# Kernel optimization log

Measured on AMD Instinct MI355X. Metric: run time of the kernel, lower is better.

## Reference

```python
import jax, jax.numpy as jnp
import numpy as np

B, S, C = 4, 2048, 2048
D = C // 4  # head dim = 512

def setup_inputs() -> dict:
    key = jax.random.key(0)
    k1, k2, k3, k4, k5 = jax.random.split(key, 5)
    scale = 1.0 / np.sqrt(C)
    return {
        "x": jax.random.normal(k1, (B, S, C), dtype=jnp.float32),
        "Wqkv": jax.random.normal(k2, (3 * D, C), dtype=jnp.float32) * scale,
        "bqkv": jax.random.normal(k3, (3 * D,), dtype=jnp.float32) * 0.01,
        "Wo": jax.random.normal(k4, (C, D), dtype=jnp.float32) * (1.0 / np.sqrt(D)),
        "bo": jax.random.normal(k5, (C,), dtype=jnp.float32) * 0.01,
    }

def reference(x, Wqkv, bqkv, Wo, bo):
    Bx, Sx, Cx = x.shape
    d = Cx // 4
    # fused QKV projection: [B,S,3d] -> split into q,k,v each [B,S,d]
    qkv = jnp.einsum('bsc,oc->bso', x, Wqkv) + bqkv
    qkv = qkv.reshape(Bx, Sx, 3, d)
    q, k, v = qkv[:, :, 0], qkv[:, :, 1], qkv[:, :, 2]
    # scaled dot-product attention (full [B,S,S] scores, as in original)
    attn = jnp.einsum('bqd,bkd->bqk', q, k) / jnp.sqrt(jnp.asarray(d, x.dtype))
    attn = jax.nn.softmax(attn, axis=-1)
    ctx = jnp.einsum('bqk,bkd->bqd', attn, v)
    # output projection d -> C
    return jnp.einsum('bsd,od->bso', ctx, Wo) + bo
```

## Files before the change

kernel.cpp:

```cpp
#include <hip/hip_runtime.h>
#include <math.h>


typedef __bf16 bf16;
typedef bf16 bf16x8 __attribute__((ext_vector_type(8)));
typedef bf16 bf16x4 __attribute__((ext_vector_type(4)));
typedef float f32x4 __attribute__((ext_vector_type(4)));

#define BB 4
#define SS 2048
#define CC 2048
#define DD 512
#define ND3 1536
#define MM 8192

typedef const __attribute__((address_space(1))) unsigned int g_u32;
typedef __attribute__((address_space(3))) unsigned int l_u32;

__device__ __forceinline__ void gl_lds16(const bf16* g, bf16* l) {
    __builtin_amdgcn_global_load_lds((g_u32*)g, (l_u32*)l, 16, 0, 0);
}

#define VMW(n) asm volatile("s_waitcnt vmcnt(" #n ")" ::: "memory")
#define BAR    __builtin_amdgcn_s_barrier()

__device__ __forceinline__ void xcd_swz(int& bx, int& by, int& bz) {
    const int gx = gridDim.x, gy = gridDim.y;
    const int nwg = gx * gy * gridDim.z;
    const int d = (blockIdx.z * gy + blockIdx.y) * gx + blockIdx.x;
    const int s = (d & 7) * (nwg >> 3) + (d >> 3);
    bx = s % gx;
    const int t2 = s / gx;
    by = t2 % gy;
    bz = t2 / gy;
}

#define N4_X   (MM * CC / 4)
#define N4_WQ  (ND3 * CC / 4)
#define N4_WO  (CC * DD / 4)
#define N4_RS  (MM / 4)
#define N4_TOT (N4_X + N4_WQ + N4_WO + N4_RS)

__global__ __launch_bounds__(256) void prep(const float* __restrict__ x,
                                            const float* __restrict__ Wqkv,
                                            const float* __restrict__ Wo,
                                            bf16* __restrict__ xb,
                                            bf16* __restrict__ wqkvb,
                                            bf16* __restrict__ wob,
                                            float* __restrict__ rsum) {
    int i = blockIdx.x * 256 + threadIdx.x;
    const int stride = gridDim.x * 256;
    for (; i < N4_TOT; i += stride) {
        if (i < N4_X + N4_WQ + N4_WO) {
            const float* src; bf16* dst; int j = i;
            if (j < N4_X)                { src = x;    dst = xb; }
            else if (j < N4_X + N4_WQ)   { src = Wqkv; dst = wqkvb; j -= N4_X; }
            else                         { src = Wo;   dst = wob;   j -= N4_X + N4_WQ; }
            float4 v = ((const float4*)src)[j];
            bf16x4 o;
            o[0] = (bf16)v.x; o[1] = (bf16)v.y; o[2] = (bf16)v.z; o[3] = (bf16)v.w;
            ((bf16x4*)dst)[j] = o;
        } else {
            int j = i - (N4_X + N4_WQ + N4_WO);
            ((float4*)rsum)[j] = float4{0.f, 0.f, 0.f, 0.f};
        }
    }
}

#define SLOT_E 16384
#define CH_B   8192

template <bool OUT_BF16, int EPI>
__device__ __forceinline__ void gemm256_body(const bf16* __restrict__ A,
                                             const bf16* __restrict__ Bm,
                                             const float* __restrict__ bias,
                                             float* __restrict__ rowsum,
                                             bf16* __restrict__ vTp,
                                             void* __restrict__ Cv,
                                             int K, int lda, int ldb, int ldc,
                                             long ab, long bb, long cb,
                                             float scale) {
    extern __shared__ bf16 lds[];
    int bx, by, bz;
    xcd_swz(bx, by, bz);
    A  += (size_t)bz * ab;
    Bm += (size_t)bz * bb;
    const int m0 = by * 256, n0 = bx * 256;
    const int t = threadIdx.x, lane = t & 63, w = t >> 6;
    const int wm = (w >> 2) * 128, wn = (w & 3) * 64;
    const int cl = lane & 15, q = lane >> 4;
    const int swzr = (q ^ ((cl >> 1) & 3)) * 8;
    const int srow = t >> 2;
    const int swz  = (t & 3) ^ ((t >> 3) & 3);
    const bf16* pa = A  + (size_t)(m0 + srow) * lda + swz * 8;
    const bf16* pb = Bm + (size_t)(n0 + srow) * ldb + swz * 8;
    bf16* lw = lds + w * 512;

    f32x4 acc[8][4] = {};
    const int NC = K >> 5;

    auto STAGE = [&](int j) {
        bf16* s = lw + (j & 3) * SLOT_E;
        const bf16* ga = pa + j * 32;
        const bf16* gb = pb + j * 32;
        gl_lds16(ga,                     s);
        gl_lds16(ga + (size_t)128 * lda, s + 4096);
        gl_lds16(gb,                     s + CH_B);
        gl_lds16(gb + (size_t)128 * ldb, s + CH_B + 4096);
    };
    auto FRAGS = [&](int j, bf16x8 (&af)[8], bf16x8 (&bfr)[4]) {
        const bf16* sa = lds + (j & 3) * SLOT_E + (wm + cl) * 32 + swzr;
        const bf16* sb = lds + (j & 3) * SLOT_E + CH_B + (wn + cl) * 32 + swzr;
#pragma unroll
        for (int i = 0; i < 8; i++)  af[i]  = *(const bf16x8*)(sa + i * 512);
#pragma unroll
        for (int jj = 0; jj < 4; jj++) bfr[jj] = *(const bf16x8*)(sb + jj * 512);
    };
    auto MFMAS = [&](bf16x8 (&af)[8], bf16x8 (&bfr)[4]) {
        __builtin_amdgcn_s_setprio(1);
#pragma unroll
        for (int i = 0; i < 8; i++)
#pragma unroll
            for (int jj = 0; jj < 4; jj++)
                acc[i][jj] = __builtin_amdgcn_mfma_f32_16x16x32_bf16(
                                 af[i], bfr[jj], acc[i][jj], 0, 0, 0);
        __builtin_amdgcn_s_setprio(0);
    };

    STAGE(0); STAGE(1); STAGE(2);
    VMW(8); BAR;

    for (int j = 0; j < NC - 3; ++j) {
        bf16x8 af[8], bfr[4];
        FRAGS(j, af, bfr);
        STAGE(j + 3);
        MFMAS(af, bfr);
        VMW(8); BAR;
    }
    {   bf16x8 af[8], bfr[4];
        FRAGS(NC - 3, af, bfr); MFMAS(af, bfr);
        VMW(4); BAR;
    }
    {   bf16x8 af[8], bfr[4];
        FRAGS(NC - 2, af, bfr); MFMAS(af, bfr);
        VMW(0); BAR;
    }
    {   bf16x8 af[8], bfr[4];
        FRAGS(NC - 1, af, bfr); MFMAS(af, bfr);
    }

    if constexpr (EPI == 4) {
        float cs[4] = {0.f, 0.f, 0.f, 0.f};
#pragma unroll
        for (int i = 0; i < 8; i++)
#pragma unroll
            for (int jj = 0; jj < 4; jj++) {
                int col = n0 + wn + jj * 16 + cl;
                int row = m0 + wm + i * 16 + q * 4;
                bf16x4 o;
#pragma unroll
                for (int r = 0; r < 4; r++) {
                    float e = __expf(acc[i][jj][r] * scale);
                    cs[jj] += e;
                    o[r] = (bf16)e;
                }
                *(bf16x4*)&((bf16*)Cv)[(size_t)bz * cb + (size_t)col * ldc + row] = o;
            }
#pragma unroll
        for (int jj = 0; jj < 4; jj++) {
            cs[jj] += __shfl_xor(cs[jj], 16, 64);
            cs[jj] += __shfl_xor(cs[jj], 32, 64);
        }
        if (q == 0) {
#pragma unroll
            for (int jj = 0; jj < 4; jj++)
                atomicAdd(&rowsum[(size_t)bz * SS + n0 + wn + jj * 16 + cl], cs[jj]);
        }
        return;
    }

    const bool v_block = (EPI == 3) && (n0 >= 1024);
#pragma unroll
    for (int i = 0; i < 8; i++) {
#pragma unroll
        for (int jj = 0; jj < 4; jj++) {
            int col = n0 + wn + jj * 16 + cl;
            float bvv = bias ? bias[col] : 0.0f;
            if (v_block) {
                int row = m0 + wm + i * 16 + q * 4;
                int b = row >> 11, s = row & 2047;
                bf16x4 o;
#pragma unroll
                for (int r = 0; r < 4; r++) o[r] = (bf16)(acc[i][jj][r] * scale + bvv);
                *(bf16x4*)&vTp[((size_t)b * DD + (col - 1024)) * SS + s] = o;
            } else {
#pragma unroll
                for (int r = 0; r < 4; r++) {
                    int row = m0 + wm + i * 16 + q * 4 + r;
                    float val = acc[i][jj][r] * scale + bvv;
                    if (OUT_BF16)
                        ((bf16*)Cv)[(size_t)bz * cb + (size_t)row * ldc + col] = (bf16)val;
                    else
                        ((float*)Cv)[(size_t)bz * cb + (size_t)row * ldc + col] = val;
                }
            }
        }
    }
}

__global__ __launch_bounds__(256) void k_pv(const bf16* __restrict__ A,
        const bf16* __restrict__ Bm, float* __restrict__ rowsum,
        bf16* __restrict__ Cv, int K, int lda, int ldb, int ldc,
        long ab, long bb, long cb) {
    __shared__ bf16 As[128 * 64];
    __shared__ bf16 Bs[64 * 64];
    int bx, by, bz;
    xcd_swz(bx, by, bz);
    A += (size_t)bz * ab;
    Bm += (size_t)bz * bb;
    const int m0 = by * 128, n0 = bx * 64;
    const int t = threadIdx.x, lane = t & 63, w = t >> 6;
    const int wm = w * 32, wn = 0;
    const int q = lane >> 4, cl = lane & 15;
    const int srow = lane >> 3;
    const int sblk = (lane & 7) ^ srow;
    const int scol = sblk * 8;
    const bf16* pa = A + (size_t)(m0 + w * 32 + srow) * lda + scol;
    const bf16* pb = Bm + (size_t)(n0 + w * 16 + srow) * ldb + scol;
    bf16* lA = As + (w * 32) * 64;
    bf16* lB = Bs + (w * 16) * 64;
    const int rblk0 = (q ^ (cl & 7)) * 8;
    const int rblk1 = ((4 + q) ^ (cl & 7)) * 8;

    f32x4 acc[2][4] = {};
    for (int k0 = 0; k0 < K; k0 += 64) {
#pragma unroll
        for (int n = 0; n < 4; n++)
            gl_lds16(pa + k0 + (size_t)(n * 8) * lda, lA + n * 8 * 64);
#pragma unroll
        for (int n = 0; n < 2; n++)
            gl_lds16(pb + k0 + (size_t)(n * 8) * ldb, lB + n * 8 * 64);
        __syncthreads();
#pragma unroll
        for (int h = 0; h < 2; h++) {
            const int rb = h ? rblk1 : rblk0;
            bf16x8 af[2], bfr[4];
#pragma unroll
            for (int i = 0; i < 2; i++)
                af[i] = *(const bf16x8*)&As[(wm + i * 16 + cl) * 64 + rb];
#pragma unroll
            for (int j = 0; j < 4; j++)
                bfr[j] = *(const bf16x8*)&Bs[(wn + j * 16 + cl) * 64 + rb];
#pragma unroll
            for (int i = 0; i < 2; i++)
#pragma unroll
                for (int j = 0; j < 4; j++)
                    acc[i][j] = __builtin_amdgcn_mfma_f32_16x16x32_bf16(af[i], bfr[j], acc[i][j], 0, 0, 0);
        }
        __syncthreads();
    }

    float inv[4];
#pragma unroll
    for (int j = 0; j < 4; j++)
        inv[j] = 1.0f / rowsum[(size_t)bz * SS + n0 + wn + j * 16 + cl];
#pragma unroll
    for (int i = 0; i < 2; i++)
#pragma unroll
        for (int j = 0; j < 4; j++) {
            int col = n0 + wn + j * 16 + cl;
            int row = m0 + wm + i * 16 + q * 4;
            bf16x4 o;
#pragma unroll
            for (int r = 0; r < 4; r++) o[r] = (bf16)(acc[i][j][r] * inv[j]);
            *(bf16x4*)&Cv[(size_t)bz * cb + (size_t)col * ldc + row] = o;
        }
}

__global__ __launch_bounds__(512, 2) void k_qkv(const bf16* A, const bf16* Bm,
        const float* bias, bf16* vTp, void* Cv, int K, int lda, int ldb, int ldc,
        float scale) {
    gemm256_body<true, 3>(A, Bm, bias, nullptr, vTp, Cv, K, lda, ldb, ldc, 0, 0, 0, scale);
}
__global__ __launch_bounds__(512, 2) void k_score(const bf16* A, const bf16* Bm,
        float* rowsum, void* Cv, int K, int lda, int ldb, int ldc,
        long ab, long bb, long cb, float scale) {
    gemm256_body<true, 4>(A, Bm, nullptr, rowsum, nullptr, Cv, K, lda, ldb, ldc, ab, bb, cb, scale);
}
__global__ __launch_bounds__(512, 2) void k_out(const bf16* A, const bf16* Bm,
        const float* bias, void* Cv, int K, int lda, int ldb, int ldc,
        float scale) {
    gemm256_body<false, 0>(A, Bm, bias, nullptr, nullptr, Cv, K, lda, ldb, ldc, 0, 0, 0, scale);
}

extern "C" void kernel_launch(void* const* d_in, const int* in_sizes, int n_in,
                              void* d_out, int out_size, void* d_ws, size_t ws_size,
                              hipStream_t stream) {
    const float* x    = (const float*)d_in[0];
    const float* Wqkv = (const float*)d_in[1];
    const float* bqkv = (const float*)d_in[2];
    const float* Wo   = (const float*)d_in[3];
    const float* bo   = (const float*)d_in[4];
    float* out = (float*)d_out;

    char* ws = (char*)d_ws;
    size_t off = 0;
    bf16* xb    = (bf16*)(ws + off); off += (size_t)MM * CC * 2;
    bf16* wqkvb = (bf16*)(ws + off); off += (size_t)ND3 * CC * 2;
    bf16* wob   = (bf16*)(ws + off); off += (size_t)CC * DD * 2;
    bf16* qkvb  = (bf16*)(ws + off); off += (size_t)MM * ND3 * 2;
    bf16* vT    = (bf16*)(ws + off); off += (size_t)BB * DD * SS * 2;
    bf16* expS  = (bf16*)(ws + off); off += (size_t)BB * SS * SS * 2;
    bf16* ctxb  = (bf16*)(ws + off); off += (size_t)MM * DD * 2;
    float* rsum = (float*)(ws + off); off += (size_t)MM * 4;

    static int lds_attr_set = 0;
    if (!lds_attr_set) {
        hipFuncSetAttribute((const void*)k_qkv,
                            hipFuncAttributeMaxDynamicSharedMemorySize, 131072);
        hipFuncSetAttribute((const void*)k_score,
                            hipFuncAttributeMaxDynamicSharedMemorySize, 131072);
        hipFuncSetAttribute((const void*)k_out,
                            hipFuncAttributeMaxDynamicSharedMemorySize, 131072);
        lds_attr_set = 1;
    }

    prep<<<2048, 256, 0, stream>>>(x, Wqkv, Wo, xb, wqkvb, wob, rsum);

    k_qkv<<<dim3(ND3 / 256, MM / 256, 1), 512, 131072, stream>>>(
        xb, wqkvb, bqkv, vT, qkvb, CC, CC, CC, ND3, 1.0f);

    k_score<<<dim3(SS / 256, SS / 256, BB), 512, 131072, stream>>>(
        qkvb + 512 , qkvb , rsum, expS,
        DD, ND3, ND3, SS,
        (long)SS * ND3, (long)SS * ND3, (long)SS * SS,
        0.044194173824159216f );

    k_pv<<<dim3(SS / 64, DD / 128, BB), 256, 0, stream>>>(
        vT, expS, rsum, ctxb,
        SS, SS, SS, DD,
        (long)DD * SS, (long)SS * SS, (long)SS * DD);

    k_out<<<dim3(CC / 256, MM / 256, 1), 512, 131072, stream>>>(
        ctxb, wob, bo, out, DD, DD, DD, CC, 1.0f);

    (void)in_sizes; (void)n_in; (void)out_size; (void)ws_size;
}
```

Baseline: 273.4 us.

## Shrink shared GEMM body to 128x128 tiles and reuse it for PV

Replaces the 256x256, 512-thread, 4-slot GEMM body with a 128x128, 256-thread body that uses a 3-slot static LDS ring. The separate k_pv kernel is dropped and PV now runs through the shared pipelined body, with a new epilogue that normalizes by the row sum. The smaller tiles give more blocks and less LDS per block, which should help occupancy and wave balance for the small QKV and output GEMMs. In exchange, each tile reuses its loaded data less and moves more global bytes per FLOP in the large GEMMs.

Result: no change. 276.8 us (+1.3%).

```diff
diff --git a/kernel.cpp b/kernel.cpp
--- a/kernel.cpp
+++ b/kernel.cpp
@@ -67,11 +67,10 @@
     }
 }
 
-#define SLOT_E 16384
-#define CH_B   8192
+#define SLOT3 8192
 
 template <bool OUT_BF16, int EPI>
-__device__ __forceinline__ void gemm256_body(const bf16* __restrict__ A,
+__device__ __forceinline__ void gemm128_body(const bf16* __restrict__ A,
                                              const bf16* __restrict__ Bm,
                                              const float* __restrict__ bias,
                                              float* __restrict__ rowsum,
@@ -80,14 +79,14 @@
                                              int K, int lda, int ldb, int ldc,
                                              long ab, long bb, long cb,
                                              float scale) {
-    extern __shared__ bf16 lds[];
+    __shared__ bf16 lds[3 * SLOT3];
     int bx, by, bz;
     xcd_swz(bx, by, bz);
     A  += (size_t)bz * ab;
     Bm += (size_t)bz * bb;
-    const int m0 = by * 256, n0 = bx * 256;
+    const int m0 = by * 128, n0 = bx * 128;
     const int t = threadIdx.x, lane = t & 63, w = t >> 6;
-    const int wm = (w >> 2) * 128, wn = (w & 3) * 64;
+    const int wm = (w >> 1) * 64, wn = (w & 1) * 64;
     const int cl = lane & 15, q = lane >> 4;
     const int swzr = (q ^ ((cl >> 1) & 3)) * 8;
     const int srow = t >> 2;
@@ -96,30 +95,30 @@
     const bf16* pb = Bm + (size_t)(n0 + srow) * ldb + swz * 8;
     bf16* lw = lds + w * 512;
 
-    f32x4 acc[8][4] = {};
+    f32x4 acc[4][4] = {};
     const int NC = K >> 5;
 
-    auto STAGE = [&](int j) {
-        bf16* s = lw + (j & 3) * SLOT_E;
+    auto STAGE = [&](int j, int sl) {
+        bf16* s = lw + sl * SLOT3;
         const bf16* ga = pa + j * 32;
         const bf16* gb = pb + j * 32;
-        gl_lds16(ga,                     s);
-        gl_lds16(ga + (size_t)128 * lda, s + 4096);
-        gl_lds16(gb,                     s + CH_B);
-        gl_lds16(gb + (size_t)128 * ldb, s + CH_B + 4096);
+        gl_lds16(ga,                    s);
+        gl_lds16(ga + (size_t)64 * lda, s + 2048);
+        gl_lds16(gb,                    s + 4096);
+        gl_lds16(gb + (size_t)64 * ldb, s + 4096 + 2048);
     };
-    auto FRAGS = [&](int j, bf16x8 (&af)[8], bf16x8 (&bfr)[4]) {
-        const bf16* sa = lds + (j & 3) * SLOT_E + (wm + cl) * 32 + swzr;
-        const bf16* sb = lds + (j & 3) * SLOT_E + CH_B + (wn + cl) * 32 + swzr;
-#pragma unroll
-        for (int i = 0; i < 8; i++)  af[i]  = *(const bf16x8*)(sa + i * 512);
+    auto FRAGS = [&](int sl, bf16x8 (&af)[4], bf16x8 (&bfr)[4]) {
+        const bf16* sa = lds + sl * SLOT3 + (wm + cl) * 32 + swzr;
+        const bf16* sb = lds + sl * SLOT3 + 4096 + (wn + cl) * 32 + swzr;
+#pragma unroll
+        for (int i = 0; i < 4; i++)  af[i]  = *(const bf16x8*)(sa + i * 512);
 #pragma unroll
         for (int jj = 0; jj < 4; jj++) bfr[jj] = *(const bf16x8*)(sb + jj * 512);
     };
-    auto MFMAS = [&](bf16x8 (&af)[8], bf16x8 (&bfr)[4]) {
+    auto MFMAS = [&](bf16x8 (&af)[4], bf16x8 (&bfr)[4]) {
         __builtin_amdgcn_s_setprio(1);
 #pragma unroll
-        for (int i = 0; i < 8; i++)
+        for (int i = 0; i < 4; i++)
 #pragma unroll
             for (int jj = 0; jj < 4; jj++)
                 acc[i][jj] = __builtin_amdgcn_mfma_f32_16x16x32_bf16(
@@ -127,32 +126,32 @@
         __builtin_amdgcn_s_setprio(0);
     };
 
-    STAGE(0); STAGE(1); STAGE(2);
-    VMW(8); BAR;
-
-    for (int j = 0; j < NC - 3; ++j) {
-        bf16x8 af[8], bfr[4];
-        FRAGS(j, af, bfr);
-        STAGE(j + 3);
+    STAGE(0, 0); STAGE(1, 1);
+    VMW(4); BAR;
+
+    int rd = 0, st = 2;
+    for (int j = 0; j < NC - 2; ++j) {
+        bf16x8 af[4], bfr[4];
+        FRAGS(rd, af, bfr);
+        STAGE(j + 2, st);
         MFMAS(af, bfr);
-        VMW(8); BAR;
-    }
-    {   bf16x8 af[8], bfr[4];
-        FRAGS(NC - 3, af, bfr); MFMAS(af, bfr);
         VMW(4); BAR;
-    }
-    {   bf16x8 af[8], bfr[4];
-        FRAGS(NC - 2, af, bfr); MFMAS(af, bfr);
+        rd = (rd == 2) ? 0 : rd + 1;
+        st = (st == 2) ? 0 : st + 1;
+    }
+    {   bf16x8 af[4], bfr[4];
+        FRAGS(rd, af, bfr); MFMAS(af, bfr);
         VMW(0); BAR;
-    }
-    {   bf16x8 af[8], bfr[4];
-        FRAGS(NC - 1, af, bfr); MFMAS(af, bfr);
+        rd = (rd == 2) ? 0 : rd + 1;
+    }
+    {   bf16x8 af[4], bfr[4];
+        FRAGS(rd, af, bfr); MFMAS(af, bfr);
     }
 
     if constexpr (EPI == 4) {
         float cs[4] = {0.f, 0.f, 0.f, 0.f};
 #pragma unroll
-        for (int i = 0; i < 8; i++)
+        for (int i = 0; i < 4; i++)
 #pragma unroll
             for (int jj = 0; jj < 4; jj++) {
                 int col = n0 + wn + jj * 16 + cl;
@@ -179,9 +178,28 @@
         return;
     }
 
+    if constexpr (EPI == 5) {
+        float inv[4];
+#pragma unroll
+        for (int jj = 0; jj < 4; jj++)
+            inv[jj] = 1.0f / rowsum[(size_t)bz * SS + n0 + wn + jj * 16 + cl];
+#pragma unroll
+        for (int i = 0; i < 4; i++)
+#pragma unroll
+            for (int jj = 0; jj < 4; jj++) {
+                int col = n0 + wn + jj * 16 + cl;
+                int row = m0 + wm + i * 16 + q * 4;
+                bf16x4 o;
+#pragma unroll
+                for (int r = 0; r < 4; r++) o[r] = (bf16)(acc[i][jj][r] * inv[jj]);
+                *(bf16x4*)&((bf16*)Cv)[(size_t)bz * cb + (size_t)col * ldc + row] = o;
+            }
+        return;
+    }
+
     const bool v_block = (EPI == 3) && (n0 >= 1024);
 #pragma unroll
-    for (int i = 0; i < 8; i++) {
+    for (int i = 0; i < 4; i++) {
 #pragma unroll
         for (int jj = 0; jj < 4; jj++) {
             int col = n0 + wn + jj * 16 + cl;
@@ -208,89 +226,25 @@
     }
 }
 
-__global__ __launch_bounds__(256) void k_pv(const bf16* __restrict__ A,
-        const bf16* __restrict__ Bm, float* __restrict__ rowsum,
-        bf16* __restrict__ Cv, int K, int lda, int ldb, int ldc,
-        long ab, long bb, long cb) {
-    __shared__ bf16 As[128 * 64];
-    __shared__ bf16 Bs[64 * 64];
-    int bx, by, bz;
-    xcd_swz(bx, by, bz);
-    A += (size_t)bz * ab;
-    Bm += (size_t)bz * bb;
-    const int m0 = by * 128, n0 = bx * 64;
-    const int t = threadIdx.x, lane = t & 63, w = t >> 6;
-    const int wm = w * 32, wn = 0;
-    const int q = lane >> 4, cl = lane & 15;
-    const int srow = lane >> 3;
-    const int sblk = (lane & 7) ^ srow;
-    const int scol = sblk * 8;
-    const bf16* pa = A + (size_t)(m0 + w * 32 + srow) * lda + scol;
-    const bf16* pb = Bm + (size_t)(n0 + w * 16 + srow) * ldb + scol;
-    bf16* lA = As + (w * 32) * 64;
-    bf16* lB = Bs + (w * 16) * 64;
-    const int rblk0 = (q ^ (cl & 7)) * 8;
-    const int rblk1 = ((4 + q) ^ (cl & 7)) * 8;
-
-    f32x4 acc[2][4] = {};
-    for (int k0 = 0; k0 < K; k0 += 64) {
-#pragma unroll
-        for (int n = 0; n < 4; n++)
-            gl_lds16(pa + k0 + (size_t)(n * 8) * lda, lA + n * 8 * 64);
-#pragma unroll
-        for (int n = 0; n < 2; n++)
-            gl_lds16(pb + k0 + (size_t)(n * 8) * ldb, lB + n * 8 * 64);
-        __syncthreads();
-#pragma unroll
-        for (int h = 0; h < 2; h++) {
-            const int rb = h ? rblk1 : rblk0;
-            bf16x8 af[2], bfr[4];
-#pragma unroll
-            for (int i = 0; i < 2; i++)
-                af[i] = *(const bf16x8*)&As[(wm + i * 16 + cl) * 64 + rb];
-#pragma unroll
-            for (int j = 0; j < 4; j++)
-                bfr[j] = *(const bf16x8*)&Bs[(wn + j * 16 + cl) * 64 + rb];
-#pragma unroll
-            for (int i = 0; i < 2; i++)
-#pragma unroll
-                for (int j = 0; j < 4; j++)
-                    acc[i][j] = __builtin_amdgcn_mfma_f32_16x16x32_bf16(af[i], bfr[j], acc[i][j], 0, 0, 0);
-        }
-        __syncthreads();
-    }
-
-    float inv[4];
-#pragma unroll
-    for (int j = 0; j < 4; j++)
-        inv[j] = 1.0f / rowsum[(size_t)bz * SS + n0 + wn + j * 16 + cl];
-#pragma unroll
-    for (int i = 0; i < 2; i++)
-#pragma unroll
-        for (int j = 0; j < 4; j++) {
-            int col = n0 + wn + j * 16 + cl;
-            int row = m0 + wm + i * 16 + q * 4;
-            bf16x4 o;
-#pragma unroll
-            for (int r = 0; r < 4; r++) o[r] = (bf16)(acc[i][j][r] * inv[j]);
-            *(bf16x4*)&Cv[(size_t)bz * cb + (size_t)col * ldc + row] = o;
-        }
-}
-
-__global__ __launch_bounds__(512, 2) void k_qkv(const bf16* A, const bf16* Bm,
+__global__ __launch_bounds__(256, 2) void k_qkv(const bf16* A, const bf16* Bm,
         const float* bias, bf16* vTp, void* Cv, int K, int lda, int ldb, int ldc,
         float scale) {
-    gemm256_body<true, 3>(A, Bm, bias, nullptr, vTp, Cv, K, lda, ldb, ldc, 0, 0, 0, scale);
-}
-__global__ __launch_bounds__(512, 2) void k_score(const bf16* A, const bf16* Bm,
+    gemm128_body<true, 3>(A, Bm, bias, nullptr, vTp, Cv, K, lda, ldb, ldc, 0, 0, 0, scale);
+}
+__global__ __launch_bounds__(256, 2) void k_score(const bf16* A, const bf16* Bm,
         float* rowsum, void* Cv, int K, int lda, int ldb, int ldc,
         long ab, long bb, long cb, float scale) {
-    gemm256_body<true, 4>(A, Bm, nullptr, rowsum, nullptr, Cv, K, lda, ldb, ldc, ab, bb, cb, scale);
-}
-__global__ __launch_bounds__(512, 2) void k_out(const bf16* A, const bf16* Bm,
+    gemm128_body<true, 4>(A, Bm, nullptr, rowsum, nullptr, Cv, K, lda, ldb, ldc, ab, bb, cb, scale);
+}
+__global__ __launch_bounds__(256, 2) void k_pv(const bf16* A, const bf16* Bm,
+        float* rowsum, void* Cv, int K, int lda, int ldb, int ldc,
+        long ab, long bb, long cb) {
+    gemm128_body<true, 5>(A, Bm, nullptr, rowsum, nullptr, Cv, K, lda, ldb, ldc, ab, bb, cb, 1.0f);
+}
+__global__ __launch_bounds__(256, 2) void k_out(const bf16* A, const bf16* Bm,
         const float* bias, void* Cv, int K, int lda, int ldb, int ldc,
         float scale) {
-    gemm256_body<false, 0>(A, Bm, bias, nullptr, nullptr, Cv, K, lda, ldb, ldc, 0, 0, 0, scale);
+    gemm128_body<false, 0>(A, Bm, bias, nullptr, nullptr, Cv, K, lda, ldb, ldc, 0, 0, 0, scale);
 }
 
 extern "C" void kernel_launch(void* const* d_in, const int* in_sizes, int n_in,
@@ -314,34 +268,23 @@
     bf16* ctxb  = (bf16*)(ws + off); off += (size_t)MM * DD * 2;
     float* rsum = (float*)(ws + off); off += (size_t)MM * 4;
 
-    static int lds_attr_set = 0;
-    if (!lds_attr_set) {
-        hipFuncSetAttribute((const void*)k_qkv,
-                            hipFuncAttributeMaxDynamicSharedMemorySize, 131072);
-        hipFuncSetAttribute((const void*)k_score,
-                            hipFuncAttributeMaxDynamicSharedMemorySize, 131072);
-        hipFuncSetAttribute((const void*)k_out,
-                            hipFuncAttributeMaxDynamicSharedMemorySize, 131072);
-        lds_attr_set = 1;
-    }
-
     prep<<<2048, 256, 0, stream>>>(x, Wqkv, Wo, xb, wqkvb, wob, rsum);
 
-    k_qkv<<<dim3(ND3 / 256, MM / 256, 1), 512, 131072, stream>>>(
+    k_qkv<<<dim3(ND3 / 128, MM / 128, 1), 256, 0, stream>>>(
         xb, wqkvb, bqkv, vT, qkvb, CC, CC, CC, ND3, 1.0f);
 
-    k_score<<<dim3(SS / 256, SS / 256, BB), 512, 131072, stream>>>(
+    k_score<<<dim3(SS / 128, SS / 128, BB), 256, 0, stream>>>(
         qkvb + 512 , qkvb , rsum, expS,
         DD, ND3, ND3, SS,
         (long)SS * ND3, (long)SS * ND3, (long)SS * SS,
         0.044194173824159216f );
 
-    k_pv<<<dim3(SS / 64, DD / 128, BB), 256, 0, stream>>>(
+    k_pv<<<dim3(SS / 128, DD / 128, BB), 256, 0, stream>>>(
         vT, expS, rsum, ctxb,
         SS, SS, SS, DD,
         (long)DD * SS, (long)SS * SS, (long)SS * DD);
 
-    k_out<<<dim3(CC / 256, MM / 256, 1), 512, 131072, stream>>>(
+    k_out<<<dim3(CC / 128, MM / 128, 1), 256, 0, stream>>>(
         ctxb, wob, bo, out, DD, DD, DD, CC, 1.0f);
 
     (void)in_sizes; (void)n_in; (void)out_size; (void)ws_size;
```
